# Performance work log

Measured on AMD Instinct MI355X. Metric: run time of the kernel, lower is better.

The kernel has to match this reference:

```python
import jax, jax.numpy as jnp
import numpy as np

N = 100000      # nodes
E = 1600000     # edges (avg degree 16)
IN, H, EMB = 64, 128, 64
G = 64          # graphs in the batch


def _w(key, shape, fan_in):
    return jax.random.normal(key, shape, jnp.float32) * (1.0 / np.sqrt(fan_in))


def setup_inputs() -> dict:
    key = jax.random.key(0)
    ks = jax.random.split(key, 16)
    x = jax.random.normal(ks[0], (N, IN), jnp.float32)
    edge_index = jax.random.randint(ks[1], (2, E), 0, N, dtype=jnp.int64)
    batch = jnp.sort(jax.random.randint(ks[2], (N,), 0, G, dtype=jnp.int64))
    return {
        "x": x,
        "edge_index": edge_index,
        "batch": batch,
        # SAGEConv 1: lin_l acts on aggregated neighbors, lin_r on the root node
        "Wl1": _w(ks[3], (IN, H), IN), "Wr1": _w(ks[4], (IN, H), IN), "b1": jnp.zeros((H,), jnp.float32),
        "Wl2": _w(ks[5], (H, H), H), "Wr2": _w(ks[6], (H, H), H), "b2": jnp.zeros((H,), jnp.float32),
        "Wl3": _w(ks[7], (H, H), H), "Wr3": _w(ks[8], (H, H), H), "b3": jnp.zeros((H,), jnp.float32),
        "W_lin1": _w(ks[9], (H, H // 2), H), "b_lin1": jnp.zeros((H // 2,), jnp.float32),
        "W_lin2": _w(ks[10], (H // 2, EMB), H // 2), "b_lin2": jnp.zeros((EMB,), jnp.float32),
    }


def _sage_conv(x, src, dst, Wl, Wr, b):
    # mean-aggregate source features onto destination nodes
    msg_sum = jax.ops.segment_sum(x[src], dst, num_segments=N)          # [N, d]
    deg = jax.ops.segment_sum(jnp.ones((src.shape[0],), x.dtype), dst, num_segments=N)
    mean = msg_sum / jnp.clip(deg, 1.0)[:, None]
    return mean @ Wl + x @ Wr + b


def _forward(x, edge_index, batch,
             Wl1, Wr1, b1, Wl2, Wr2, b2, Wl3, Wr3, b3,
             W_lin1, b_lin1, W_lin2, b_lin2):
    src, dst = edge_index[0], edge_index[1]
    h = jax.nn.relu(_sage_conv(x, src, dst, Wl1, Wr1, b1))
    h = jax.nn.relu(_sage_conv(h, src, dst, Wl2, Wr2, b2))
    h = jax.nn.relu(_sage_conv(h, src, dst, Wl3, Wr3, b3))
    # global mean pool per graph
    pooled = jax.ops.segment_sum(h, batch, num_segments=G)              # [G, H]
    counts = jax.ops.segment_sum(jnp.ones((N,), h.dtype), batch, num_segments=G)
    pooled = pooled / jnp.clip(counts, 1.0)[:, None]
    h = jax.nn.relu(pooled @ W_lin1 + b_lin1)
    # dropout p=0.5 is identity in eval mode
    return h @ W_lin2 + b_lin2


def reference(x, edge_index, batch,
              Wl1, Wr1, b1, Wl2, Wr2, b2, Wl3, Wr3, b3,
              W_lin1, b_lin1, W_lin2, b_lin2):
    return _forward(x, edge_index, batch, Wl1, Wr1, b1, Wl2, Wr2, b2,
                    Wl3, Wr3, b3, W_lin1, b_lin1, W_lin2, b_lin2)
```

## Files before the change

kernel.cpp:

```cpp
#include <hip/hip_runtime.h>
#include <hip/hip_bf16.h>
#include <cstdint>
#include <cstddef>

#define NN 100000
#define NE 1600000
#define NG 64
#define NPAD 100096
#define NBUK 782
#define CAP 3072
#define NFB 256
#define CHUNK 6250

typedef short short8v __attribute__((ext_vector_type(8)));
typedef float float4v __attribute__((ext_vector_type(4)));
typedef float float2v __attribute__((ext_vector_type(2)));


__device__ __forceinline__ int lower_bound_i(const int* __restrict__ a, int n, int v) {
  int lo = 0, hi = n;
  while (lo < hi) { int m = (lo + hi) >> 1; if (a[m] < v) lo = m + 1; else hi = m; }
  return lo;
}

__device__ __forceinline__ float bf2f(ushort u) {
  return __uint_as_float(((unsigned int)u) << 16);
}

__device__ __forceinline__ float bflo(unsigned int u) {
  return __uint_as_float(u << 16);
}
__device__ __forceinline__ float bfhi(unsigned int u) {
  return __uint_as_float(u & 0xffff0000u);
}

__device__ __forceinline__ ushort f2bf(float f) {
  __hip_bfloat16 h = __float2bfloat16(f);
  return *reinterpret_cast<ushort*>(&h);
}

__device__ __forceinline__ unsigned int pack_bf16x2(float2v v) {
  return (unsigned int)f2bf(v.x) | ((unsigned int)f2bf(v.y) << 16);
}

template <bool HI>
__device__ __forceinline__ unsigned int pk_fp8(float a, float b, unsigned int old) {
  return (unsigned int)__builtin_amdgcn_cvt_pk_fp8_f32(a, b, (int)old, HI);
}


__global__ void pack_x_kernel(const float* __restrict__ x, ushort* __restrict__ xb,
                              unsigned int* __restrict__ x8, int* __restrict__ bcur) {
  int i4 = blockIdx.x * blockDim.x + threadIdx.x;
  if (i4 < NBUK) bcur[i4] = i4 * CAP;
  int idx = i4 * 4;
  if (idx >= NN * 64) return;
  float4 v = *(const float4*)(x + idx);
  ushort4 o;
  o.x = f2bf(v.x); o.y = f2bf(v.y); o.z = f2bf(v.z); o.w = f2bf(v.w);
  *(ushort4*)(xb + idx) = o;
  unsigned int r = pk_fp8<false>(v.x, v.y, 0u);
  r = pk_fp8<true>(v.z, v.w, r);
  x8[i4] = r;
}

__device__ __forceinline__ void pack_one(const float* __restrict__ Wl,
                                         const float* __restrict__ Wr,
                                         ushort* __restrict__ Wp, int K, int idx) {
  int lane = idx & 63;
  int ft   = (idx >> 6) & 7;
  int kkp  = idx >> 9;
  int kbase = kkp * 32 + (lane >> 4) * 8;
  int isR = kbase >= K;
  const float* W = isR ? Wr : Wl;
  int k0 = kbase - (isR ? K : 0);
  int colf = ft * 16 + (lane & 15);
  ushort4 lo, hi;
  lo.x = f2bf(W[(k0 + 0) * 128 + colf]);
  lo.y = f2bf(W[(k0 + 1) * 128 + colf]);
  lo.z = f2bf(W[(k0 + 2) * 128 + colf]);
  lo.w = f2bf(W[(k0 + 3) * 128 + colf]);
  hi.x = f2bf(W[(k0 + 4) * 128 + colf]);
  hi.y = f2bf(W[(k0 + 5) * 128 + colf]);
  hi.z = f2bf(W[(k0 + 6) * 128 + colf]);
  hi.w = f2bf(W[(k0 + 7) * 128 + colf]);
  *(ushort4*)(Wp + (size_t)idx * 8)     = lo;
  *(ushort4*)(Wp + (size_t)idx * 8 + 4) = hi;
}

__global__ void pack_w_all_kernel(const float* __restrict__ Wl1, const float* __restrict__ Wr1,
                                  ushort* __restrict__ wp1,
                                  const float* __restrict__ Wl2, const float* __restrict__ Wr2,
                                  ushort* __restrict__ wp2,
                                  const float* __restrict__ Wl3, const float* __restrict__ Wr3,
                                  ushort* __restrict__ wp3) {
  int idx = blockIdx.x * blockDim.x + threadIdx.x;
  if (idx < 2048)       pack_one(Wl1, Wr1, wp1, 64,  idx);
  else if (idx < 6144)  pack_one(Wl2, Wr2, wp2, 128, idx - 2048);
  else if (idx < 10240) pack_one(Wl3, Wr3, wp3, 128, idx - 6144);
}


__global__ __launch_bounds__(1024) void bucket_fill_kernel(const int* __restrict__ src,
                                                           const int* __restrict__ dst,
                                                           int* __restrict__ bcur,
                                                           unsigned int* __restrict__ bp) {
  __shared__ int lhist[NBUK];
  __shared__ int lbase[NBUK];
  int tid = threadIdx.x;
  int e0 = blockIdx.x * CHUNK;
  int e1 = e0 + CHUNK;
  for (int i = tid; i < NBUK; i += 1024) lhist[i] = 0;
  __syncthreads();
  for (int i = e0 + tid; i < e1; i += 1024) atomicAdd(&lhist[dst[i] >> 7], 1);
  __syncthreads();
  for (int b = tid; b < NBUK; b += 1024) {
    int c = lhist[b];
    lbase[b] = c ? atomicAdd(&bcur[b], c) : 0;
    lhist[b] = 0;
  }
  __syncthreads();
  for (int i = e0 + tid; i < e1; i += 1024) {
    int d = dst[i];
    int b = d >> 7;
    int p = atomicAdd(&lhist[b], 1);
    int pos = lbase[b] + p;
    if (pos < (b + 1) * CAP)
      bp[pos] = ((unsigned int)(d & 127) << 17) | (unsigned int)src[i];
  }
}

__global__ __launch_bounds__(1024) void bucket_scan_kernel(const int* __restrict__ bcur,
                                                           int* __restrict__ boff,
                                                           int* __restrict__ rs,
                                                           float* __restrict__ pooled) {
  __shared__ int wsum[16];
  int tid = threadIdx.x, lane = tid & 63, wid = tid >> 6;
  int v = 0;
  if (tid < NBUK) v = min(bcur[tid] - tid * CAP, CAP);
  int incl = v;
  #pragma unroll
  for (int off = 1; off < 64; off <<= 1) {
    int t = __shfl_up(incl, off, 64);
    if (lane >= off) incl += t;
  }
  if (lane == 63) wsum[wid] = incl;
  __syncthreads();
  if (tid == 0) {
    int acc = 0;
    #pragma unroll
    for (int j = 0; j < 16; ++j) { int t = wsum[j]; wsum[j] = acc; acc += t; }
  }
  __syncthreads();
  int excl = incl - v + wsum[wid];
  if (tid <= NBUK) boff[tid] = excl;
  for (int i = tid; i < NG * 128; i += 1024) pooled[i] = 0.f;
  if (tid == 0) rs[NN] = NE;
}

__global__ __launch_bounds__(256) void bucket_csr_kernel(const unsigned int* __restrict__ bp,
                                                         const int* __restrict__ boff,
                                                         int* __restrict__ rs,
                                                         int* __restrict__ col) {
  __shared__ int sdeg[128], sinc[128], lcur[128];
  int b = blockIdx.x, tid = threadIdx.x;
  int n0 = b << 7;
  int e0 = boff[b], e1 = boff[b + 1];
  int cnt = e1 - e0;
  const unsigned int* __restrict__ mybp = bp + (size_t)b * CAP;
  if (tid < 128) sdeg[tid] = 0;
  __syncthreads();
  for (int i = tid; i < cnt; i += 256) atomicAdd(&sdeg[mybp[i] >> 17], 1);
  __syncthreads();
  if (tid < 128) sinc[tid] = sdeg[tid];
  __syncthreads();
  #pragma unroll
  for (int off = 1; off < 128; off <<= 1) {
    int add = 0;
    if (tid < 128 && tid >= off) add = sinc[tid - off];
    __syncthreads();
    if (tid < 128) sinc[tid] += add;
    __syncthreads();
  }
  if (tid < 128) {
    int excl = sinc[tid] - sdeg[tid];
    lcur[tid] = excl;
    int node = n0 + tid;
    if (node < NN) rs[node] = e0 + excl;
  }
  __syncthreads();
  for (int i = tid; i < cnt; i += 256) {
    unsigned int v = mybp[i];
    int p = atomicAdd(&lcur[v >> 17], 1);
    col[e0 + p] = (int)(v & 0x1FFFF);
  }
}


__global__ __launch_bounds__(256) void agg128_kernel(const unsigned int* __restrict__ X8,
                                                     const int* __restrict__ rs,
                                                     const int* __restrict__ col,
                                                     unsigned int* __restrict__ out, int n) {
  int t = threadIdx.x;
  int fl = t & 7;
  int node = blockIdx.x * 32 + (t >> 3);
  if (node >= n) return;
  int a = rs[node], b = rs[node + 1];
  const unsigned int* __restrict__ Xc = X8 + fl * 4;
  float2v acc[8];
  #pragma unroll
  for (int j = 0; j < 8; ++j) acc[j] = (float2v){0.f, 0.f};
  int j = a;
  for (; j + 1 < b; j += 2) {
    int s0 = col[j];
    int s1 = col[j + 1];
    uint4 u0 = *(const uint4*)(Xc + (size_t)s0 * 32);
    uint4 u1 = *(const uint4*)(Xc + (size_t)s1 * 32);
    acc[0] += __builtin_amdgcn_cvt_pk_f32_fp8(u0.x, false);
    acc[1] += __builtin_amdgcn_cvt_pk_f32_fp8(u0.x, true);
    acc[2] += __builtin_amdgcn_cvt_pk_f32_fp8(u0.y, false);
    acc[3] += __builtin_amdgcn_cvt_pk_f32_fp8(u0.y, true);
    acc[4] += __builtin_amdgcn_cvt_pk_f32_fp8(u0.z, false);
    acc[5] += __builtin_amdgcn_cvt_pk_f32_fp8(u0.z, true);
    acc[6] += __builtin_amdgcn_cvt_pk_f32_fp8(u0.w, false);
    acc[7] += __builtin_amdgcn_cvt_pk_f32_fp8(u0.w, true);
    acc[0] += __builtin_amdgcn_cvt_pk_f32_fp8(u1.x, false);
    acc[1] += __builtin_amdgcn_cvt_pk_f32_fp8(u1.x, true);
    acc[2] += __builtin_amdgcn_cvt_pk_f32_fp8(u1.y, false);
    acc[3] += __builtin_amdgcn_cvt_pk_f32_fp8(u1.y, true);
    acc[4] += __builtin_amdgcn_cvt_pk_f32_fp8(u1.z, false);
    acc[5] += __builtin_amdgcn_cvt_pk_f32_fp8(u1.z, true);
    acc[6] += __builtin_amdgcn_cvt_pk_f32_fp8(u1.w, false);
    acc[7] += __builtin_amdgcn_cvt_pk_f32_fp8(u1.w, true);
  }
  if (j < b) {
    int s = col[j];
    uint4 u = *(const uint4*)(Xc + (size_t)s * 32);
    acc[0] += __builtin_amdgcn_cvt_pk_f32_fp8(u.x, false);
    acc[1] += __builtin_amdgcn_cvt_pk_f32_fp8(u.x, true);
    acc[2] += __builtin_amdgcn_cvt_pk_f32_fp8(u.y, false);
    acc[3] += __builtin_amdgcn_cvt_pk_f32_fp8(u.y, true);
    acc[4] += __builtin_amdgcn_cvt_pk_f32_fp8(u.z, false);
    acc[5] += __builtin_amdgcn_cvt_pk_f32_fp8(u.z, true);
    acc[6] += __builtin_amdgcn_cvt_pk_f32_fp8(u.w, false);
    acc[7] += __builtin_amdgcn_cvt_pk_f32_fp8(u.w, true);
  }
  int d = b - a;
  float inv = d > 0 ? 1.0f / (float)d : 0.f;
  float2v iv = (float2v){inv, inv};
  uint4 o0, o1;
  o0.x = pack_bf16x2(acc[0] * iv); o0.y = pack_bf16x2(acc[1] * iv);
  o0.z = pack_bf16x2(acc[2] * iv); o0.w = pack_bf16x2(acc[3] * iv);
  o1.x = pack_bf16x2(acc[4] * iv); o1.y = pack_bf16x2(acc[5] * iv);
  o1.z = pack_bf16x2(acc[6] * iv); o1.w = pack_bf16x2(acc[7] * iv);
  unsigned int* op = out + (size_t)node * 64 + fl * 8;
  *(uint4*)op = o0;
  *(uint4*)(op + 4) = o1;
}

__global__ __launch_bounds__(256) void agg64_kernel(const unsigned int* __restrict__ X8,
                                                    const int* __restrict__ rs,
                                                    const int* __restrict__ col,
                                                    unsigned int* __restrict__ out, int n) {
  int t = threadIdx.x;
  int fl = t & 7;
  int node = blockIdx.x * 32 + (t >> 3);
  if (node >= n) return;
  int a = rs[node], b = rs[node + 1];
  const unsigned int* __restrict__ Xc = X8 + fl * 2;
  float2v acc[4];
  #pragma unroll
  for (int j = 0; j < 4; ++j) acc[j] = (float2v){0.f, 0.f};
  int j = a;
  for (; j + 1 < b; j += 2) {
    int s0 = col[j];
    int s1 = col[j + 1];
    uint2 u0 = *(const uint2*)(Xc + (size_t)s0 * 16);
    uint2 u1 = *(const uint2*)(Xc + (size_t)s1 * 16);
    acc[0] += __builtin_amdgcn_cvt_pk_f32_fp8(u0.x, false);
    acc[1] += __builtin_amdgcn_cvt_pk_f32_fp8(u0.x, true);
    acc[2] += __builtin_amdgcn_cvt_pk_f32_fp8(u0.y, false);
    acc[3] += __builtin_amdgcn_cvt_pk_f32_fp8(u0.y, true);
    acc[0] += __builtin_amdgcn_cvt_pk_f32_fp8(u1.x, false);
    acc[1] += __builtin_amdgcn_cvt_pk_f32_fp8(u1.x, true);
    acc[2] += __builtin_amdgcn_cvt_pk_f32_fp8(u1.y, false);
    acc[3] += __builtin_amdgcn_cvt_pk_f32_fp8(u1.y, true);
  }
  if (j < b) {
    int s = col[j];
    uint2 u = *(const uint2*)(Xc + (size_t)s * 16);
    acc[0] += __builtin_amdgcn_cvt_pk_f32_fp8(u.x, false);
    acc[1] += __builtin_amdgcn_cvt_pk_f32_fp8(u.x, true);
    acc[2] += __builtin_amdgcn_cvt_pk_f32_fp8(u.y, false);
    acc[3] += __builtin_amdgcn_cvt_pk_f32_fp8(u.y, true);
  }
  int d = b - a;
  float inv = d > 0 ? 1.0f / (float)d : 0.f;
  float2v iv = (float2v){inv, inv};
  uint4 o;
  o.x = pack_bf16x2(acc[0] * iv); o.y = pack_bf16x2(acc[1] * iv);
  o.z = pack_bf16x2(acc[2] * iv); o.w = pack_bf16x2(acc[3] * iv);
  *(uint4*)(out + (size_t)node * 32 + fl * 4) = o;
}


template <int K>
__global__ __launch_bounds__(256) void mfma_gemm_kernel(const ushort* __restrict__ Mean,
                                                        const ushort* __restrict__ Xb,
                                                        const ushort* __restrict__ Wp,
                                                        const float* __restrict__ bias,
                                                        ushort* __restrict__ Out,
                                                        unsigned int* __restrict__ Out8) {
  constexpr int KS = K / 32;
  int lane = threadIdx.x & 63;
  int wave = threadIdx.x >> 6;
  int quad = lane >> 4;
  int l16  = lane & 15;
  size_t node0 = (size_t)blockIdx.x * 128 + wave * 32;

  float4v acc[2][8];
  #pragma unroll
  for (int g = 0; g < 2; ++g)
    #pragma unroll
    for (int ft = 0; ft < 8; ++ft)
      acc[g][ft] = (float4v){0.f, 0.f, 0.f, 0.f};

  #pragma unroll
  for (int s = 0; s < 2; ++s) {
    const ushort* __restrict__ A = s ? Xb : Mean;
    #pragma unroll
    for (int kk = 0; kk < KS; ++kk) {
      int kkp = s * KS + kk;
      short8v wv[8];
      const ushort* wb = Wp + ((size_t)(kkp * 8) * 64 + lane) * 8;
      #pragma unroll
      for (int ft = 0; ft < 8; ++ft)
        wv[ft] = *(const short8v*)(wb + (size_t)ft * 64 * 8);
      short8v av[2];
      #pragma unroll
      for (int g = 0; g < 2; ++g)
        av[g] = *(const short8v*)(A + (node0 + g * 16 + l16) * K + kk * 32 + quad * 8);
      #pragma unroll
      for (int g = 0; g < 2; ++g)
        #pragma unroll
        for (int ft = 0; ft < 8; ++ft)
          acc[g][ft] = __builtin_amdgcn_mfma_f32_16x16x32_bf16(wv[ft], av[g], acc[g][ft], 0, 0, 0);
    }
  }

  #pragma unroll
  for (int g = 0; g < 2; ++g) {
    size_t nrow = node0 + g * 16 + l16;
    #pragma unroll
    for (int ft = 0; ft < 8; ++ft) {
      float4 bb = *(const float4*)(bias + ft * 16 + quad * 4);
      float4v v = acc[g][ft];
      float r0 = fmaxf(v.x + bb.x, 0.f);
      float r1 = fmaxf(v.y + bb.y, 0.f);
      float r2 = fmaxf(v.z + bb.z, 0.f);
      float r3 = fmaxf(v.w + bb.w, 0.f);
      ushort4 o;
      o.x = f2bf(r0); o.y = f2bf(r1); o.z = f2bf(r2); o.w = f2bf(r3);
      *(ushort4*)(Out + nrow * 128 + ft * 16 + quad * 4) = o;
      if (Out8) {
        unsigned int r = pk_fp8<false>(r0, r1, 0u);
        r = pk_fp8<true>(r2, r3, r);
        Out8[nrow * 32 + ft * 4 + quad] = r;
      }
    }
  }
}


__global__ __launch_bounds__(256) void pool_kernel(const unsigned int* __restrict__ H,
                                                   const int* __restrict__ batch,
                                                   float* __restrict__ pooled) {
  __shared__ float part[4][128];
  int t = threadIdx.x;
  int fl = t & 15;
  int sub = t >> 4;
  int n0 = blockIdx.x * 128;
  for (int i = t; i < 512; i += 256) ((float*)part)[i] = 0.f;
  int g0 = batch[n0];
  __syncthreads();
  float acc[8];
  #pragma unroll
  for (int j = 0; j < 8; ++j) acc[j] = 0.f;
  int curgi = 0;
  for (int i = 0; i < 8; ++i) {
    int node = n0 + sub + 16 * i;
    if (node >= NN) break;
    int gi = batch[node] - g0;
    if (gi != curgi) {
      if (curgi < 4) {
        #pragma unroll
        for (int j = 0; j < 8; ++j) {
          if (acc[j] != 0.f) atomicAdd(&part[curgi][fl * 8 + j], acc[j]);
          acc[j] = 0.f;
        }
      }
      curgi = gi;
    }
    uint4 u = *(const uint4*)(H + (size_t)node * 64 + fl * 4);
    if (curgi < 4) {
      acc[0] += bflo(u.x); acc[1] += bfhi(u.x);
      acc[2] += bflo(u.y); acc[3] += bfhi(u.y);
      acc[4] += bflo(u.z); acc[5] += bfhi(u.z);
      acc[6] += bflo(u.w); acc[7] += bfhi(u.w);
    } else {
      float* pg = &pooled[(g0 + gi) * 128 + fl * 8];
      atomicAdd(&pg[0], bflo(u.x)); atomicAdd(&pg[1], bfhi(u.x));
      atomicAdd(&pg[2], bflo(u.y)); atomicAdd(&pg[3], bfhi(u.y));
      atomicAdd(&pg[4], bflo(u.z)); atomicAdd(&pg[5], bfhi(u.z));
      atomicAdd(&pg[6], bflo(u.w)); atomicAdd(&pg[7], bfhi(u.w));
    }
  }
  if (curgi < 4) {
    #pragma unroll
    for (int j = 0; j < 8; ++j)
      if (acc[j] != 0.f) atomicAdd(&part[curgi][fl * 8 + j], acc[j]);
  }
  __syncthreads();
  int nlast = min(n0 + 127, NN - 1);
  int nslot = min(batch[nlast] - g0 + 1, 4);
  if (t < 128) {
    for (int s = 0; s < nslot; ++s) {
      float v = part[s][t];
      if (v != 0.f) atomicAdd(&pooled[(g0 + s) * 128 + t], v);
    }
  }
}


__global__ __launch_bounds__(64) void mlp_kernel(const float* __restrict__ pooled,
                                                 const int* __restrict__ batch,
                                                 const float* __restrict__ W1,
                                                 const float* __restrict__ b1,
                                                 const float* __restrict__ W2,
                                                 const float* __restrict__ b2,
                                                 float* __restrict__ out, int n) {
  __shared__ float p[128];
  __shared__ float h1[64];
  int g = blockIdx.x, f = threadIdx.x;
  int lo = lower_bound_i(batch, n, g);
  int hi = lower_bound_i(batch, n, g + 1);
  float inv = (hi > lo) ? 1.0f / (float)(hi - lo) : 0.f;
  p[f]      = pooled[g * 128 + f] * inv;
  p[f + 64] = pooled[g * 128 + 64 + f] * inv;
  __syncthreads();
  float a = b1[f];
  #pragma unroll 8
  for (int k = 0; k < 128; ++k) a = fmaf(p[k], W1[k * 64 + f], a);
  a = fmaxf(a, 0.f);
  h1[f] = a;
  __syncthreads();
  float o = b2[f];
  #pragma unroll 8
  for (int k = 0; k < 64; ++k) o = fmaf(h1[k], W2[k * 64 + f], o);
  out[g * 64 + f] = o;
}


extern "C" void kernel_launch(void* const* d_in, const int* in_sizes, int n_in,
                              void* d_out, int out_size, void* d_ws, size_t ws_size,
                              hipStream_t stream) {
  const float* x      = (const float*)d_in[0];
  const int*   edge   = (const int*)d_in[1];
  const int*   batch  = (const int*)d_in[2];
  const float* Wl1    = (const float*)d_in[3];
  const float* Wr1    = (const float*)d_in[4];
  const float* b1     = (const float*)d_in[5];
  const float* Wl2    = (const float*)d_in[6];
  const float* Wr2    = (const float*)d_in[7];
  const float* b2     = (const float*)d_in[8];
  const float* Wl3    = (const float*)d_in[9];
  const float* Wr3    = (const float*)d_in[10];
  const float* b3     = (const float*)d_in[11];
  const float* Wlin1  = (const float*)d_in[12];
  const float* blin1  = (const float*)d_in[13];
  const float* Wlin2  = (const float*)d_in[14];
  const float* blin2  = (const float*)d_in[15];
  float* out = (float*)d_out;

  const int* src = edge;
  const int* dst = edge + NE;

  char* ws = (char*)d_ws;
  size_t off = 0;
  auto alloc = [&](size_t bytes) -> char* {
    char* p = ws + off;
    off = (off + bytes + 255) & ~(size_t)255;
    return p;
  };
  int*    rs     = (int*)alloc((size_t)(NN + 1) * 4);
  int*    col    = (int*)alloc((size_t)NE * 4);
  int*    bcur   = (int*)alloc((size_t)NBUK * 4);
  int*    boff   = (int*)alloc((size_t)(NBUK + 1) * 4);
  unsigned int* bp = (unsigned int*)alloc((size_t)NBUK * CAP * 4);
  ushort* xb     = (ushort*)alloc((size_t)NPAD * 64 * 2);
  unsigned int* x8 = (unsigned int*)alloc((size_t)NPAD * 64);
  unsigned int* h8 = (unsigned int*)alloc((size_t)NPAD * 128);
  ushort* mean64 = (ushort*)alloc((size_t)NPAD * 64 * 2);
  ushort* mean128= (ushort*)alloc((size_t)NPAD * 128 * 2);
  ushort* h1     = (ushort*)alloc((size_t)NPAD * 128 * 2);
  ushort* h2     = (ushort*)alloc((size_t)NPAD * 128 * 2);
  ushort* h3     = (ushort*)alloc((size_t)NPAD * 128 * 2);
  ushort* wp1    = (ushort*)alloc((size_t)2 * 64 * 128 * 2);
  ushort* wp2    = (ushort*)alloc((size_t)2 * 128 * 128 * 2);
  ushort* wp3    = (ushort*)alloc((size_t)2 * 128 * 128 * 2);
  float*  pooled = (float*)alloc((size_t)NG * 128 * 4);
  (void)ws_size; (void)n_in; (void)in_sizes; (void)out_size;

  pack_x_kernel<<<(NN * 64 / 4 + 255) / 256, 256, 0, stream>>>(x, xb, x8, bcur);
  pack_w_all_kernel<<<40, 256, 0, stream>>>(Wl1, Wr1, wp1, Wl2, Wr2, wp2, Wl3, Wr3, wp3);
  bucket_fill_kernel<<<NFB, 1024, 0, stream>>>(src, dst, bcur, bp);
  bucket_scan_kernel<<<1, 1024, 0, stream>>>(bcur, boff, rs, pooled);
  bucket_csr_kernel<<<NBUK, 256, 0, stream>>>(bp, boff, rs, col);

  agg64_kernel<<<(NN + 31) / 32, 256, 0, stream>>>(x8, rs, col, (unsigned int*)mean64, NN);
  mfma_gemm_kernel<64><<<NPAD / 128, 256, 0, stream>>>(mean64, xb, wp1, b1, h1, h8);

  agg128_kernel<<<(NN + 31) / 32, 256, 0, stream>>>(h8, rs, col, (unsigned int*)mean128, NN);
  mfma_gemm_kernel<128><<<NPAD / 128, 256, 0, stream>>>(mean128, h1, wp2, b2, h2, h8);

  agg128_kernel<<<(NN + 31) / 32, 256, 0, stream>>>(h8, rs, col, (unsigned int*)mean128, NN);
  mfma_gemm_kernel<128><<<NPAD / 128, 256, 0, stream>>>(mean128, h2, wp3, b3, h3, nullptr);

  pool_kernel<<<(NN + 127) / 128, 256, 0, stream>>>((const unsigned int*)h3, batch, pooled);
  mlp_kernel<<<NG, 64, 0, stream>>>(pooled, batch, Wlin1, blin1, Wlin2, blin2, out, NN);
}
```

Measured before the change: 359.9 us.

## Fuse neighbor mean aggregation into SAGE GEMM via shared-memory staging

```diff
diff --git a/kernel.cpp b/kernel.cpp
--- a/kernel.cpp
+++ b/kernel.cpp
@@ -197,123 +197,119 @@
 }
 
 
-__global__ __launch_bounds__(256) void agg128_kernel(const unsigned int* __restrict__ X8,
-                                                     const int* __restrict__ rs,
-                                                     const int* __restrict__ col,
-                                                     unsigned int* __restrict__ out, int n) {
-  int t = threadIdx.x;
-  int fl = t & 7;
-  int node = blockIdx.x * 32 + (t >> 3);
-  if (node >= n) return;
-  int a = rs[node], b = rs[node + 1];
-  const unsigned int* __restrict__ Xc = X8 + fl * 4;
-  float2v acc[8];
-  #pragma unroll
-  for (int j = 0; j < 8; ++j) acc[j] = (float2v){0.f, 0.f};
-  int j = a;
-  for (; j + 1 < b; j += 2) {
-    int s0 = col[j];
-    int s1 = col[j + 1];
-    uint4 u0 = *(const uint4*)(Xc + (size_t)s0 * 32);
-    uint4 u1 = *(const uint4*)(Xc + (size_t)s1 * 32);
-    acc[0] += __builtin_amdgcn_cvt_pk_f32_fp8(u0.x, false);
-    acc[1] += __builtin_amdgcn_cvt_pk_f32_fp8(u0.x, true);
-    acc[2] += __builtin_amdgcn_cvt_pk_f32_fp8(u0.y, false);
-    acc[3] += __builtin_amdgcn_cvt_pk_f32_fp8(u0.y, true);
-    acc[4] += __builtin_amdgcn_cvt_pk_f32_fp8(u0.z, false);
-    acc[5] += __builtin_amdgcn_cvt_pk_f32_fp8(u0.z, true);
-    acc[6] += __builtin_amdgcn_cvt_pk_f32_fp8(u0.w, false);
-    acc[7] += __builtin_amdgcn_cvt_pk_f32_fp8(u0.w, true);
-    acc[0] += __builtin_amdgcn_cvt_pk_f32_fp8(u1.x, false);
-    acc[1] += __builtin_amdgcn_cvt_pk_f32_fp8(u1.x, true);
-    acc[2] += __builtin_amdgcn_cvt_pk_f32_fp8(u1.y, false);
-    acc[3] += __builtin_amdgcn_cvt_pk_f32_fp8(u1.y, true);
-    acc[4] += __builtin_amdgcn_cvt_pk_f32_fp8(u1.z, false);
-    acc[5] += __builtin_amdgcn_cvt_pk_f32_fp8(u1.z, true);
-    acc[6] += __builtin_amdgcn_cvt_pk_f32_fp8(u1.w, false);
-    acc[7] += __builtin_amdgcn_cvt_pk_f32_fp8(u1.w, true);
-  }
-  if (j < b) {
-    int s = col[j];
-    uint4 u = *(const uint4*)(Xc + (size_t)s * 32);
-    acc[0] += __builtin_amdgcn_cvt_pk_f32_fp8(u.x, false);
-    acc[1] += __builtin_amdgcn_cvt_pk_f32_fp8(u.x, true);
-    acc[2] += __builtin_amdgcn_cvt_pk_f32_fp8(u.y, false);
-    acc[3] += __builtin_amdgcn_cvt_pk_f32_fp8(u.y, true);
-    acc[4] += __builtin_amdgcn_cvt_pk_f32_fp8(u.z, false);
-    acc[5] += __builtin_amdgcn_cvt_pk_f32_fp8(u.z, true);
-    acc[6] += __builtin_amdgcn_cvt_pk_f32_fp8(u.w, false);
-    acc[7] += __builtin_amdgcn_cvt_pk_f32_fp8(u.w, true);
-  }
-  int d = b - a;
-  float inv = d > 0 ? 1.0f / (float)d : 0.f;
-  float2v iv = (float2v){inv, inv};
-  uint4 o0, o1;
-  o0.x = pack_bf16x2(acc[0] * iv); o0.y = pack_bf16x2(acc[1] * iv);
-  o0.z = pack_bf16x2(acc[2] * iv); o0.w = pack_bf16x2(acc[3] * iv);
-  o1.x = pack_bf16x2(acc[4] * iv); o1.y = pack_bf16x2(acc[5] * iv);
-  o1.z = pack_bf16x2(acc[6] * iv); o1.w = pack_bf16x2(acc[7] * iv);
-  unsigned int* op = out + (size_t)node * 64 + fl * 8;
-  *(uint4*)op = o0;
-  *(uint4*)(op + 4) = o1;
-}
-
-__global__ __launch_bounds__(256) void agg64_kernel(const unsigned int* __restrict__ X8,
-                                                    const int* __restrict__ rs,
-                                                    const int* __restrict__ col,
-                                                    unsigned int* __restrict__ out, int n) {
-  int t = threadIdx.x;
-  int fl = t & 7;
-  int node = blockIdx.x * 32 + (t >> 3);
-  if (node >= n) return;
-  int a = rs[node], b = rs[node + 1];
-  const unsigned int* __restrict__ Xc = X8 + fl * 2;
-  float2v acc[4];
-  #pragma unroll
-  for (int j = 0; j < 4; ++j) acc[j] = (float2v){0.f, 0.f};
-  int j = a;
-  for (; j + 1 < b; j += 2) {
-    int s0 = col[j];
-    int s1 = col[j + 1];
-    uint2 u0 = *(const uint2*)(Xc + (size_t)s0 * 16);
-    uint2 u1 = *(const uint2*)(Xc + (size_t)s1 * 16);
-    acc[0] += __builtin_amdgcn_cvt_pk_f32_fp8(u0.x, false);
-    acc[1] += __builtin_amdgcn_cvt_pk_f32_fp8(u0.x, true);
-    acc[2] += __builtin_amdgcn_cvt_pk_f32_fp8(u0.y, false);
-    acc[3] += __builtin_amdgcn_cvt_pk_f32_fp8(u0.y, true);
-    acc[0] += __builtin_amdgcn_cvt_pk_f32_fp8(u1.x, false);
-    acc[1] += __builtin_amdgcn_cvt_pk_f32_fp8(u1.x, true);
-    acc[2] += __builtin_amdgcn_cvt_pk_f32_fp8(u1.y, false);
-    acc[3] += __builtin_amdgcn_cvt_pk_f32_fp8(u1.y, true);
-  }
-  if (j < b) {
-    int s = col[j];
-    uint2 u = *(const uint2*)(Xc + (size_t)s * 16);
-    acc[0] += __builtin_amdgcn_cvt_pk_f32_fp8(u.x, false);
-    acc[1] += __builtin_amdgcn_cvt_pk_f32_fp8(u.x, true);
-    acc[2] += __builtin_amdgcn_cvt_pk_f32_fp8(u.y, false);
-    acc[3] += __builtin_amdgcn_cvt_pk_f32_fp8(u.y, true);
-  }
-  int d = b - a;
-  float inv = d > 0 ? 1.0f / (float)d : 0.f;
-  float2v iv = (float2v){inv, inv};
-  uint4 o;
-  o.x = pack_bf16x2(acc[0] * iv); o.y = pack_bf16x2(acc[1] * iv);
-  o.z = pack_bf16x2(acc[2] * iv); o.w = pack_bf16x2(acc[3] * iv);
-  *(uint4*)(out + (size_t)node * 32 + fl * 4) = o;
-}
-
-
 template <int K>
-__global__ __launch_bounds__(256) void mfma_gemm_kernel(const ushort* __restrict__ Mean,
-                                                        const ushort* __restrict__ Xb,
-                                                        const ushort* __restrict__ Wp,
-                                                        const float* __restrict__ bias,
-                                                        ushort* __restrict__ Out,
-                                                        unsigned int* __restrict__ Out8) {
+__global__ __launch_bounds__(256) void sage_fused_kernel(
+    const unsigned int* __restrict__ X8,
+    const int* __restrict__ rs,
+    const int* __restrict__ col,
+    const ushort* __restrict__ Xb,
+    const ushort* __restrict__ Wp,
+    const float* __restrict__ bias,
+    ushort* __restrict__ Out,
+    unsigned int* __restrict__ Out8) {
   constexpr int KS = K / 32;
+  constexpr int RW = K + 8;
+  __shared__ ushort lmean[128 * RW];
   int lane = threadIdx.x & 63;
   int wave = threadIdx.x >> 6;
+
+  {
+    int fl = lane & 7;
+    const unsigned int* __restrict__ Xc = X8 + fl * (K / 32);
+    #pragma unroll
+    for (int p = 0; p < 4; ++p) {
+      int nloc = wave * 32 + p * 8 + (lane >> 3);
+      int node = blockIdx.x * 128 + nloc;
+      ushort* lrow = lmean + nloc * RW + fl * (K / 8);
+      if (node >= NN) {
+        uint4 z = make_uint4(0, 0, 0, 0);
+        *(uint4*)lrow = z;
+        if constexpr (K == 128) *(uint4*)(lrow + 8) = z;
+      } else {
+        int a = rs[node], b = rs[node + 1];
+        float inv = (b > a) ? 1.0f / (float)(b - a) : 0.f;
+        float2v iv = (float2v){inv, inv};
+        if constexpr (K == 128) {
+          float2v acc[8];
+          #pragma unroll
+          for (int q = 0; q < 8; ++q) acc[q] = (float2v){0.f, 0.f};
+          int j = a;
+          for (; j + 1 < b; j += 2) {
+            int s0 = col[j], s1 = col[j + 1];
+            uint4 u0 = *(const uint4*)(Xc + (size_t)s0 * 32);
+            uint4 u1 = *(const uint4*)(Xc + (size_t)s1 * 32);
+            acc[0] += __builtin_amdgcn_cvt_pk_f32_fp8(u0.x, false);
+            acc[1] += __builtin_amdgcn_cvt_pk_f32_fp8(u0.x, true);
+            acc[2] += __builtin_amdgcn_cvt_pk_f32_fp8(u0.y, false);
+            acc[3] += __builtin_amdgcn_cvt_pk_f32_fp8(u0.y, true);
+            acc[4] += __builtin_amdgcn_cvt_pk_f32_fp8(u0.z, false);
+            acc[5] += __builtin_amdgcn_cvt_pk_f32_fp8(u0.z, true);
+            acc[6] += __builtin_amdgcn_cvt_pk_f32_fp8(u0.w, false);
+            acc[7] += __builtin_amdgcn_cvt_pk_f32_fp8(u0.w, true);
+            acc[0] += __builtin_amdgcn_cvt_pk_f32_fp8(u1.x, false);
+            acc[1] += __builtin_amdgcn_cvt_pk_f32_fp8(u1.x, true);
+            acc[2] += __builtin_amdgcn_cvt_pk_f32_fp8(u1.y, false);
+            acc[3] += __builtin_amdgcn_cvt_pk_f32_fp8(u1.y, true);
+            acc[4] += __builtin_amdgcn_cvt_pk_f32_fp8(u1.z, false);
+            acc[5] += __builtin_amdgcn_cvt_pk_f32_fp8(u1.z, true);
+            acc[6] += __builtin_amdgcn_cvt_pk_f32_fp8(u1.w, false);
+            acc[7] += __builtin_amdgcn_cvt_pk_f32_fp8(u1.w, true);
+          }
+          if (j < b) {
+            int s = col[j];
+            uint4 u = *(const uint4*)(Xc + (size_t)s * 32);
+            acc[0] += __builtin_amdgcn_cvt_pk_f32_fp8(u.x, false);
+            acc[1] += __builtin_amdgcn_cvt_pk_f32_fp8(u.x, true);
+            acc[2] += __builtin_amdgcn_cvt_pk_f32_fp8(u.y, false);
+            acc[3] += __builtin_amdgcn_cvt_pk_f32_fp8(u.y, true);
+            acc[4] += __builtin_amdgcn_cvt_pk_f32_fp8(u.z, false);
+            acc[5] += __builtin_amdgcn_cvt_pk_f32_fp8(u.z, true);
+            acc[6] += __builtin_amdgcn_cvt_pk_f32_fp8(u.w, false);
+            acc[7] += __builtin_amdgcn_cvt_pk_f32_fp8(u.w, true);
+          }
+          uint4 o0, o1;
+          o0.x = pack_bf16x2(acc[0] * iv); o0.y = pack_bf16x2(acc[1] * iv);
+          o0.z = pack_bf16x2(acc[2] * iv); o0.w = pack_bf16x2(acc[3] * iv);
+          o1.x = pack_bf16x2(acc[4] * iv); o1.y = pack_bf16x2(acc[5] * iv);
+          o1.z = pack_bf16x2(acc[6] * iv); o1.w = pack_bf16x2(acc[7] * iv);
+          *(uint4*)lrow = o0;
+          *(uint4*)(lrow + 8) = o1;
+        } else {
+          float2v acc[4];
+          #pragma unroll
+          for (int q = 0; q < 4; ++q) acc[q] = (float2v){0.f, 0.f};
+          int j = a;
+          for (; j + 1 < b; j += 2) {
+            int s0 = col[j], s1 = col[j + 1];
+            uint2 u0 = *(const uint2*)(Xc + (size_t)s0 * 16);
+            uint2 u1 = *(const uint2*)(Xc + (size_t)s1 * 16);
+            acc[0] += __builtin_amdgcn_cvt_pk_f32_fp8(u0.x, false);
+            acc[1] += __builtin_amdgcn_cvt_pk_f32_fp8(u0.x, true);
+            acc[2] += __builtin_amdgcn_cvt_pk_f32_fp8(u0.y, false);
+            acc[3] += __builtin_amdgcn_cvt_pk_f32_fp8(u0.y, true);
+            acc[0] += __builtin_amdgcn_cvt_pk_f32_fp8(u1.x, false);
+            acc[1] += __builtin_amdgcn_cvt_pk_f32_fp8(u1.x, true);
+            acc[2] += __builtin_amdgcn_cvt_pk_f32_fp8(u1.y, false);
+            acc[3] += __builtin_amdgcn_cvt_pk_f32_fp8(u1.y, true);
+          }
+          if (j < b) {
+            int s = col[j];
+            uint2 u = *(const uint2*)(Xc + (size_t)s * 16);
+            acc[0] += __builtin_amdgcn_cvt_pk_f32_fp8(u.x, false);
+            acc[1] += __builtin_amdgcn_cvt_pk_f32_fp8(u.x, true);
+            acc[2] += __builtin_amdgcn_cvt_pk_f32_fp8(u.y, false);
+            acc[3] += __builtin_amdgcn_cvt_pk_f32_fp8(u.y, true);
+          }
+          uint4 o;
+          o.x = pack_bf16x2(acc[0] * iv); o.y = pack_bf16x2(acc[1] * iv);
+          o.z = pack_bf16x2(acc[2] * iv); o.w = pack_bf16x2(acc[3] * iv);
+          *(uint4*)lrow = o;
+        }
+      }
+    }
+  }
+  __syncthreads();
+
   int quad = lane >> 4;
   int l16  = lane & 15;
   size_t node0 = (size_t)blockIdx.x * 128 + wave * 32;
@@ -327,7 +323,6 @@
 
   #pragma unroll
   for (int s = 0; s < 2; ++s) {
-    const ushort* __restrict__ A = s ? Xb : Mean;
     #pragma unroll
     for (int kk = 0; kk < KS; ++kk) {
       int kkp = s * KS + kk;
@@ -338,8 +333,12 @@
         wv[ft] = *(const short8v*)(wb + (size_t)ft * 64 * 8);
       short8v av[2];
       #pragma unroll
-      for (int g = 0; g < 2; ++g)
-        av[g] = *(const short8v*)(A + (node0 + g * 16 + l16) * K + kk * 32 + quad * 8);
+      for (int g = 0; g < 2; ++g) {
+        int nloc = wave * 32 + g * 16 + l16;
+        av[g] = (s == 0)
+          ? *(const short8v*)(lmean + nloc * RW + kk * 32 + quad * 8)
+          : *(const short8v*)(Xb + ((size_t)blockIdx.x * 128 + nloc) * K + kk * 32 + quad * 8);
+      }
       #pragma unroll
       for (int g = 0; g < 2; ++g)
         #pragma unroll
@@ -498,10 +497,9 @@
   int*    boff   = (int*)alloc((size_t)(NBUK + 1) * 4);
   unsigned int* bp = (unsigned int*)alloc((size_t)NBUK * CAP * 4);
   ushort* xb     = (ushort*)alloc((size_t)NPAD * 64 * 2);
-  unsigned int* x8 = (unsigned int*)alloc((size_t)NPAD * 64);
-  unsigned int* h8 = (unsigned int*)alloc((size_t)NPAD * 128);
-  ushort* mean64 = (ushort*)alloc((size_t)NPAD * 64 * 2);
-  ushort* mean128= (ushort*)alloc((size_t)NPAD * 128 * 2);
+  unsigned int* x8  = (unsigned int*)alloc((size_t)NPAD * 64);
+  unsigned int* h8a = (unsigned int*)alloc((size_t)NPAD * 128);
+  unsigned int* h8b = (unsigned int*)alloc((size_t)NPAD * 128);
   ushort* h1     = (ushort*)alloc((size_t)NPAD * 128 * 2);
   ushort* h2     = (ushort*)alloc((size_t)NPAD * 128 * 2);
   ushort* h3     = (ushort*)alloc((size_t)NPAD * 128 * 2);
@@ -517,14 +515,9 @@
   bucket_scan_kernel<<<1, 1024, 0, stream>>>(bcur, boff, rs, pooled);
   bucket_csr_kernel<<<NBUK, 256, 0, stream>>>(bp, boff, rs, col);
 
-  agg64_kernel<<<(NN + 31) / 32, 256, 0, stream>>>(x8, rs, col, (unsigned int*)mean64, NN);
-  mfma_gemm_kernel<64><<<NPAD / 128, 256, 0, stream>>>(mean64, xb, wp1, b1, h1, h8);
-
-  agg128_kernel<<<(NN + 31) / 32, 256, 0, stream>>>(h8, rs, col, (unsigned int*)mean128, NN);
-  mfma_gemm_kernel<128><<<NPAD / 128, 256, 0, stream>>>(mean128, h1, wp2, b2, h2, h8);
-
-  agg128_kernel<<<(NN + 31) / 32, 256, 0, stream>>>(h8, rs, col, (unsigned int*)mean128, NN);
-  mfma_gemm_kernel<128><<<NPAD / 128, 256, 0, stream>>>(mean128, h2, wp3, b3, h3, nullptr);
+  sage_fused_kernel<64><<<NPAD / 128, 256, 0, stream>>>(x8, rs, col, xb, wp1, b1, h1, h8a);
+  sage_fused_kernel<128><<<NPAD / 128, 256, 0, stream>>>(h8a, rs, col, h1, wp2, b2, h2, h8b);
+  sage_fused_kernel<128><<<NPAD / 128, 256, 0, stream>>>(h8b, rs, col, h2, wp3, b3, h3, nullptr);
 
   pool_kernel<<<(NN + 127) / 128, 256, 0, stream>>>((const unsigned int*)h3, batch, pooled);
   mlp_kernel<<<NG, 64, 0, stream>>>(pooled, batch, Wlin1, blin1, Wlin2, blin2, out, NN);
```

Measured after the change: 442.2 us. 22.9% more time.

## Fuse global mean pooling into last SAGE layer GEMM epilogue

Applied to the files above, without the earlier changes.

```diff
diff --git a/kernel.cpp b/kernel.cpp
--- a/kernel.cpp
+++ b/kernel.cpp
@@ -304,19 +304,28 @@
 }
 
 
-template <int K>
+template <int K, bool POOL>
 __global__ __launch_bounds__(256) void mfma_gemm_kernel(const ushort* __restrict__ Mean,
                                                         const ushort* __restrict__ Xb,
                                                         const ushort* __restrict__ Wp,
                                                         const float* __restrict__ bias,
                                                         ushort* __restrict__ Out,
-                                                        unsigned int* __restrict__ Out8) {
+                                                        unsigned int* __restrict__ Out8,
+                                                        const int* __restrict__ batch,
+                                                        float* __restrict__ pooled) {
   constexpr int KS = K / 32;
+  __shared__ float part[2][128];
   int lane = threadIdx.x & 63;
   int wave = threadIdx.x >> 6;
   int quad = lane >> 4;
   int l16  = lane & 15;
   size_t node0 = (size_t)blockIdx.x * 128 + wave * 32;
+  int g0b = 0;
+  if constexpr (POOL) {
+    ((float*)part)[threadIdx.x] = 0.f;
+    g0b = batch[blockIdx.x * 128];
+    __syncthreads();
+  }
 
   float4v acc[2][8];
   #pragma unroll
@@ -351,6 +360,7 @@
   #pragma unroll
   for (int g = 0; g < 2; ++g) {
     size_t nrow = node0 + g * 16 + l16;
+    int nf = (int)node0 + g * 16;
     #pragma unroll
     for (int ft = 0; ft < 8; ++ft) {
       float4 bb = *(const float4*)(bias + ft * 16 + quad * 4);
@@ -359,74 +369,68 @@
       float r1 = fmaxf(v.y + bb.y, 0.f);
       float r2 = fmaxf(v.z + bb.z, 0.f);
       float r3 = fmaxf(v.w + bb.w, 0.f);
-      ushort4 o;
-      o.x = f2bf(r0); o.y = f2bf(r1); o.z = f2bf(r2); o.w = f2bf(r3);
-      *(ushort4*)(Out + nrow * 128 + ft * 16 + quad * 4) = o;
-      if (Out8) {
-        unsigned int r = pk_fp8<false>(r0, r1, 0u);
-        r = pk_fp8<true>(r2, r3, r);
-        Out8[nrow * 32 + ft * 4 + quad] = r;
+      if constexpr (POOL) {
+        int fbase = ft * 16 + quad * 4;
+        bool fast = (nf + 15 < NN) && (batch[nf] == batch[nf + 15]);
+        if (fast) {
+          float s0 = r0, s1 = r1, s2 = r2, s3 = r3;
+          #pragma unroll
+          for (int off = 1; off < 16; off <<= 1) {
+            s0 += __shfl_xor(s0, off, 64);
+            s1 += __shfl_xor(s1, off, 64);
+            s2 += __shfl_xor(s2, off, 64);
+            s3 += __shfl_xor(s3, off, 64);
+          }
+          if (l16 == 0) {
+            int slot = batch[nf] - g0b;
+            if (slot < 2) {
+              atomicAdd(&part[slot][fbase + 0], s0);
+              atomicAdd(&part[slot][fbase + 1], s1);
+              atomicAdd(&part[slot][fbase + 2], s2);
+              atomicAdd(&part[slot][fbase + 3], s3);
+            } else {
+              float* pg = &pooled[batch[nf] * 128 + fbase];
+              atomicAdd(pg + 0, s0); atomicAdd(pg + 1, s1);
+              atomicAdd(pg + 2, s2); atomicAdd(pg + 3, s3);
+            }
+          }
+        } else {
+          int node = nf + l16;
+          if (node < NN) {
+            int slot = batch[node] - g0b;
+            if (slot < 2) {
+              atomicAdd(&part[slot][fbase + 0], r0);
+              atomicAdd(&part[slot][fbase + 1], r1);
+              atomicAdd(&part[slot][fbase + 2], r2);
+              atomicAdd(&part[slot][fbase + 3], r3);
+            } else {
+              float* pg = &pooled[batch[node] * 128 + fbase];
+              atomicAdd(pg + 0, r0); atomicAdd(pg + 1, r1);
+              atomicAdd(pg + 2, r2); atomicAdd(pg + 3, r3);
+            }
+          }
+        }
+      } else {
+        ushort4 o;
+        o.x = f2bf(r0); o.y = f2bf(r1); o.z = f2bf(r2); o.w = f2bf(r3);
+        *(ushort4*)(Out + nrow * 128 + ft * 16 + quad * 4) = o;
+        if (Out8) {
+          unsigned int r = pk_fp8<false>(r0, r1, 0u);
+          r = pk_fp8<true>(r2, r3, r);
+          Out8[nrow * 32 + ft * 4 + quad] = r;
+        }
       }
     }
   }
-}
-
-
-__global__ __launch_bounds__(256) void pool_kernel(const unsigned int* __restrict__ H,
-                                                   const int* __restrict__ batch,
-                                                   float* __restrict__ pooled) {
-  __shared__ float part[4][128];
-  int t = threadIdx.x;
-  int fl = t & 15;
-  int sub = t >> 4;
-  int n0 = blockIdx.x * 128;
-  for (int i = t; i < 512; i += 256) ((float*)part)[i] = 0.f;
-  int g0 = batch[n0];
-  __syncthreads();
-  float acc[8];
-  #pragma unroll
-  for (int j = 0; j < 8; ++j) acc[j] = 0.f;
-  int curgi = 0;
-  for (int i = 0; i < 8; ++i) {
-    int node = n0 + sub + 16 * i;
-    if (node >= NN) break;
-    int gi = batch[node] - g0;
-    if (gi != curgi) {
-      if (curgi < 4) {
-        #pragma unroll
-        for (int j = 0; j < 8; ++j) {
-          if (acc[j] != 0.f) atomicAdd(&part[curgi][fl * 8 + j], acc[j]);
-          acc[j] = 0.f;
-        }
+
+  if constexpr (POOL) {
+    __syncthreads();
+    if (threadIdx.x < 128) {
+      #pragma unroll
+      for (int s = 0; s < 2; ++s) {
+        float v = part[s][threadIdx.x];
+        if (v != 0.f) atomicAdd(&pooled[(g0b + s) * 128 + threadIdx.x], v);
       }
-      curgi = gi;
-    }
-    uint4 u = *(const uint4*)(H + (size_t)node * 64 + fl * 4);
-    if (curgi < 4) {
-      acc[0] += bflo(u.x); acc[1] += bfhi(u.x);
-      acc[2] += bflo(u.y); acc[3] += bfhi(u.y);
-      acc[4] += bflo(u.z); acc[5] += bfhi(u.z);
-      acc[6] += bflo(u.w); acc[7] += bfhi(u.w);
-    } else {
-      float* pg = &pooled[(g0 + gi) * 128 + fl * 8];
-      atomicAdd(&pg[0], bflo(u.x)); atomicAdd(&pg[1], bfhi(u.x));
-      atomicAdd(&pg[2], bflo(u.y)); atomicAdd(&pg[3], bfhi(u.y));
-      atomicAdd(&pg[4], bflo(u.z)); atomicAdd(&pg[5], bfhi(u.z));
-      atomicAdd(&pg[6], bflo(u.w)); atomicAdd(&pg[7], bfhi(u.w));
-    }
-  }
-  if (curgi < 4) {
-    #pragma unroll
-    for (int j = 0; j < 8; ++j)
-      if (acc[j] != 0.f) atomicAdd(&part[curgi][fl * 8 + j], acc[j]);
-  }
-  __syncthreads();
-  int nlast = min(n0 + 127, NN - 1);
-  int nslot = min(batch[nlast] - g0 + 1, 4);
-  if (t < 128) {
-    for (int s = 0; s < nslot; ++s) {
-      float v = part[s][t];
-      if (v != 0.f) atomicAdd(&pooled[(g0 + s) * 128 + t], v);
     }
   }
 }
@@ -498,13 +502,12 @@
   int*    boff   = (int*)alloc((size_t)(NBUK + 1) * 4);
   unsigned int* bp = (unsigned int*)alloc((size_t)NBUK * CAP * 4);
   ushort* xb     = (ushort*)alloc((size_t)NPAD * 64 * 2);
-  unsigned int* x8 = (unsigned int*)alloc((size_t)NPAD * 64);
-  unsigned int* h8 = (unsigned int*)alloc((size_t)NPAD * 128);
+  unsigned int* x8  = (unsigned int*)alloc((size_t)NPAD * 64);
+  unsigned int* h8  = (unsigned int*)alloc((size_t)NPAD * 128);
   ushort* mean64 = (ushort*)alloc((size_t)NPAD * 64 * 2);
   ushort* mean128= (ushort*)alloc((size_t)NPAD * 128 * 2);
   ushort* h1     = (ushort*)alloc((size_t)NPAD * 128 * 2);
   ushort* h2     = (ushort*)alloc((size_t)NPAD * 128 * 2);
-  ushort* h3     = (ushort*)alloc((size_t)NPAD * 128 * 2);
   ushort* wp1    = (ushort*)alloc((size_t)2 * 64 * 128 * 2);
   ushort* wp2    = (ushort*)alloc((size_t)2 * 128 * 128 * 2);
   ushort* wp3    = (ushort*)alloc((size_t)2 * 128 * 128 * 2);
@@ -518,14 +521,16 @@
   bucket_csr_kernel<<<NBUK, 256, 0, stream>>>(bp, boff, rs, col);
 
   agg64_kernel<<<(NN + 31) / 32, 256, 0, stream>>>(x8, rs, col, (unsigned int*)mean64, NN);
-  mfma_gemm_kernel<64><<<NPAD / 128, 256, 0, stream>>>(mean64, xb, wp1, b1, h1, h8);
+  mfma_gemm_kernel<64, false><<<NPAD / 128, 256, 0, stream>>>(mean64, xb, wp1, b1, h1, h8,
+                                                              nullptr, nullptr);
 
   agg128_kernel<<<(NN + 31) / 32, 256, 0, stream>>>(h8, rs, col, (unsigned int*)mean128, NN);
-  mfma_gemm_kernel<128><<<NPAD / 128, 256, 0, stream>>>(mean128, h1, wp2, b2, h2, h8);
+  mfma_gemm_kernel<128, false><<<NPAD / 128, 256, 0, stream>>>(mean128, h1, wp2, b2, h2, h8,
+                                                               nullptr, nullptr);
 
   agg128_kernel<<<(NN + 31) / 32, 256, 0, stream>>>(h8, rs, col, (unsigned int*)mean128, NN);
-  mfma_gemm_kernel<128><<<NPAD / 128, 256, 0, stream>>>(mean128, h2, wp3, b3, h3, nullptr);
-
-  pool_kernel<<<(NN + 127) / 128, 256, 0, stream>>>((const unsigned int*)h3, batch, pooled);
+  mfma_gemm_kernel<128, true><<<NPAD / 128, 256, 0, stream>>>(mean128, h2, wp3, b3, nullptr,
+                                                              nullptr, batch, pooled);
+
   mlp_kernel<<<NG, 64, 0, stream>>>(pooled, batch, Wlin1, blin1, Wlin2, blin2, out, NN);
 }
```

Result: faster. 346.1 us (-3.8%).
